# Kernel tuning notes

Hardware: AMD Instinct MI355X
Metric: run time of the kernel (lower is better)

Reference implementation:

```python
import jax, jax.numpy as jnp
import numpy as np

B, T, C, H = 2, 2048, 1024, 16
HS = C // H  # head size = 64


def _rope_cos_sin(t, hs):
    # theta_i = 1/10000^(2(i-1)/hs) for i in [1, hs/2]
    pos = jnp.arange(t, dtype=jnp.float32)[:, None]          # [T,1]
    i = jnp.arange(1, hs // 2 + 1, dtype=jnp.float32)[None]  # [1,hs/2]
    theta = 1.0 / 10000.0 ** (2.0 * (i - 1.0) / hs)
    ang = pos * theta                                        # [T,hs/2]
    return jnp.cos(ang), jnp.sin(ang)


def _apply_rope(u, cos, sin):
    # u: [B,H,T,HS]; complex multiply on consecutive pairs
    u2 = u.reshape(*u.shape[:-1], HS // 2, 2)
    x0, x1 = u2[..., 0], u2[..., 1]
    c = cos[None, None]  # [1,1,T,hs/2]
    s = sin[None, None]
    r0 = x0 * c - x1 * s
    r1 = x0 * s + x1 * c
    return jnp.stack([r0, r1], axis=-1).reshape(u.shape)


def setup_inputs() -> dict:
    key = jax.random.key(0)
    ks = jax.random.split(key, 5)
    return {
        "x": jax.random.normal(ks[0], (B, T, C), dtype=jnp.float32),
        "W_qkv": jax.random.normal(ks[1], (C, 3 * C), dtype=jnp.float32) * 0.02,
        "b_qkv": jax.random.normal(ks[2], (3 * C,), dtype=jnp.float32) * 0.02,
        "W_proj": jax.random.normal(ks[3], (C, C), dtype=jnp.float32) * 0.02,
        "b_proj": jax.random.normal(ks[4], (C,), dtype=jnp.float32) * 0.02,
    }


def reference(x, W_qkv, b_qkv, W_proj, b_proj):
    b, t, c = x.shape
    qkv = x @ W_qkv + b_qkv                                   # [B,T,3C]
    qkv = qkv.reshape(b, t, H, 3 * HS).transpose(0, 2, 1, 3)  # [B,H,T,3*HS]
    q, k, v = jnp.split(qkv, 3, axis=-1)                      # each [B,H,T,HS]

    cos, sin = _rope_cos_sin(t, HS)
    q = _apply_rope(q, cos, sin)
    k = _apply_rope(k, cos, sin)

    att = jnp.einsum("bhqd,bhkd->bhqk", q, k) / jnp.sqrt(jnp.float32(HS))
    causal = jnp.tril(jnp.ones((t, t), dtype=bool))[None, None]
    att = jnp.where(causal, att, jnp.float32(-1e9))
    att = jax.nn.softmax(att, axis=-1)
    y = jnp.einsum("bhqk,bhkd->bhqd", att, v)                 # [B,H,T,HS]
    y = y.transpose(0, 2, 1, 3).reshape(b, t, c)
    return y @ W_proj + b_proj
```

## Files before the change

kernel.cpp:

```cpp
#include <hip/hip_runtime.h>

typedef unsigned short u16;
typedef unsigned int u32;
typedef __bf16 bf16x8 __attribute__((ext_vector_type(8)));
typedef float f32x4 __attribute__((ext_vector_type(4)));
typedef float f32x16 __attribute__((ext_vector_type(16)));
typedef u32 u32x4 __attribute__((ext_vector_type(4)));
typedef u16 u16x4 __attribute__((ext_vector_type(4)));
typedef u16 u16x8 __attribute__((ext_vector_type(8)));

__device__ __forceinline__ u16 f2bf(float f) {
  u32 u = __builtin_bit_cast(u32, f);
  u += 0x7fffu + ((u >> 16) & 1u);
  return (u16)(u >> 16);
}

__device__ __forceinline__ u32 pk2(float a, float b) {
  u32 ua = __builtin_bit_cast(u32, a) + 0x8000u;
  u32 ub = __builtin_bit_cast(u32, b) + 0x8000u;
  return __builtin_amdgcn_perm(ub, ua, 0x07060302);
}

__device__ __forceinline__ void gld16(const void* g, void* l) {
  __builtin_amdgcn_global_load_lds(
      (const __attribute__((address_space(1))) void*)g,
      (__attribute__((address_space(3))) void*)l, 16, 0, 0);
}

__global__ __launch_bounds__(256) void k_prep(
    const float* __restrict__ x, u16* __restrict__ xb,
    const float* __restrict__ Wqkv, u16* __restrict__ Wqkvt,
    const float* __restrict__ Wproj, u16* __restrict__ Wpt,
    float2* __restrict__ rope) {
  __shared__ float tile[32][33];
  const int tid = threadIdx.x;
  int bx = blockIdx.x;
  if (bx < 4096) {
    int i = (bx * 256 + tid) * 4;
    float4 v = *(const float4*)(x + i);
    u16x4 o = { f2bf(v.x), f2bf(v.y), f2bf(v.z), f2bf(v.w) };
    *(u16x4*)(xb + i) = o;
    return;
  }
  bx -= 4096;
  const float* src; u16* dst; int R, Cc, bxx, byy;
  if (bx < 3072) {
    src = Wqkv; dst = Wqkvt; R = 1024; Cc = 3072; bxx = bx % 96; byy = bx / 96;
  } else if (bx < 4096) {
    int b = bx - 3072;
    src = Wproj; dst = Wpt; R = 1024; Cc = 1024; bxx = b % 32; byy = b / 32;
  } else {
    int i = (bx - 4096) * 256 + tid;
    int t = i >> 5, d = i & 31;
    float theta = expf(-(float)d * 0.28782313662425575f);
    float ang = (float)t * theta;
    rope[i] = make_float2(cosf(ang), sinf(ang));
    return;
  }
  int xx = tid & 31, yy = tid >> 5;
  int c0 = bxx * 32, r0 = byy * 32;
  for (int i = 0; i < 4; ++i)
    tile[yy + 8 * i][xx] = src[(size_t)(r0 + yy + 8 * i) * Cc + c0 + xx];
  __syncthreads();
  for (int i = 0; i < 4; ++i)
    dst[(size_t)(c0 + yy + 8 * i) * R + r0 + xx] = f2bf(tile[xx][yy + 8 * i]);
}

__global__ __launch_bounds__(256, 4) void k_qkv(
    const u16* __restrict__ Xb,
    const u16* __restrict__ Wt,
    const float* __restrict__ bias,
    const float2* __restrict__ rope,
    u16* __restrict__ Qg,
    u16* __restrict__ Kg,
    u16* __restrict__ Vt) {
  __shared__ alignas(16) u16 smem[18432];
  u16* As = smem;
  u16* Bs = smem + 8192;
  const int tid = threadIdx.x;
  const int lane = tid & 63, w = tid >> 6;
  const int quad = lane >> 4, l15 = lane & 15;
  const int m0 = blockIdx.y * 128, n0 = blockIdx.x * 128;
  const int wm = (w & 1) * 64, wn = (w >> 1) * 64;
  const int srow = lane >> 3, sj = lane & 7;
  const int sw = (sj ^ srow) * 8;
  const f32x4 vzero = {0.f, 0.f, 0.f, 0.f};

  f32x4 acc[4][4];
  for (int i = 0; i < 4; ++i)
    for (int j = 0; j < 4; ++j) acc[i][j] = vzero;

  for (int kt = 0; kt < 1024; kt += 64) {
    __syncthreads();
    for (int i = 0; i < 4; ++i) {
      int row = w * 32 + i * 8;
      gld16(Xb + (size_t)(m0 + row + srow) * 1024 + kt + sw, &As[row * 64]);
      gld16(Wt + (size_t)(n0 + row + srow) * 1024 + kt + sw, &Bs[row * 64]);
    }
    __syncthreads();
    for (int ks = 0; ks < 2; ++ks) {
      const int cc = ((ks * 4 + quad) ^ (l15 & 7)) * 8;
      bf16x8 a[4], b[4];
      for (int mt = 0; mt < 4; ++mt)
        a[mt] = *(const bf16x8*)&As[(wm + mt * 16 + l15) * 64 + cc];
      for (int nt = 0; nt < 4; ++nt)
        b[nt] = *(const bf16x8*)&Bs[(wn + nt * 16 + l15) * 64 + cc];
      for (int nt = 0; nt < 4; ++nt)
        for (int mt = 0; mt < 4; ++mt)
          acc[nt][mt] = __builtin_amdgcn_mfma_f32_16x16x32_bf16(
              b[nt], a[mt], acc[nt][mt], 0, 0, 0);
    }
  }
  __syncthreads();

  const int half = w >> 1;
  const int nh = n0 + half * 64;
  const int region = (nh % 192) >> 6;
  u16* Eh = smem + half * 9216;
  if (region < 2) {
    const float qsc = (region == 0) ? 0.18033688011112042f : 1.0f;
    for (int nt = 0; nt < 4; ++nt) {
      float4 bv4 = *(const float4*)&bias[nh + nt * 16 + quad * 4];
      for (int mt = 0; mt < 4; ++mt) {
        int m_l = wm + mt * 16 + l15;
        int t = (m0 + m_l) & 2047;
        float4 cs = *(const float4*)&rope[t * 32 + nt * 8 + quad * 2];
        float v0 = acc[nt][mt][0] + bv4.x;
        float v1 = acc[nt][mt][1] + bv4.y;
        float v2 = acc[nt][mt][2] + bv4.z;
        float v3 = acc[nt][mt][3] + bv4.w;
        float r0 = fmaf(-v1, cs.y, v0 * cs.x) * qsc;
        float r1 = fmaf( v0, cs.y, v1 * cs.x) * qsc;
        float r2 = fmaf(-v3, cs.w, v2 * cs.z) * qsc;
        float r3 = fmaf( v2, cs.w, v3 * cs.z) * qsc;
        uint2 pv; pv.x = pk2(r0, r1); pv.y = pk2(r2, r3);
        *(uint2*)&Eh[m_l * 72 + nt * 16 + quad * 4] = pv;
      }
    }
  } else {
    for (int nt = 0; nt < 4; ++nt) {
      float4 bv4 = *(const float4*)&bias[nh + nt * 16 + quad * 4];
      for (int mt = 0; mt < 4; ++mt) {
        int m_l = wm + mt * 16 + l15;
        int cb = nt * 16 + quad * 4;
        Eh[(cb + 0) * 136 + m_l] = f2bf(acc[nt][mt][0] + bv4.x);
        Eh[(cb + 1) * 136 + m_l] = f2bf(acc[nt][mt][1] + bv4.y);
        Eh[(cb + 2) * 136 + m_l] = f2bf(acc[nt][mt][2] + bv4.z);
        Eh[(cb + 3) * 136 + m_l] = f2bf(acc[nt][mt][3] + bv4.w);
      }
    }
  }
  __syncthreads();

  const int bb = m0 >> 11, t0 = m0 & 2047;
  for (int hf = 0; hf < 2; ++hf) {
    const int nhf = n0 + hf * 64;
    const int hh = nhf / 192;
    const int reg = (nhf % 192) >> 6;
    const u16* Ef = smem + hf * 9216;
    if (reg < 2) {
      u16* dst = (reg == 0 ? Qg : Kg) +
                 ((size_t)(bb * 16 + hh) * 2048 + t0) * 64;
      int chunk = tid & 7, row0 = tid >> 3;
      for (int p = 0; p < 4; ++p) {
        int row = row0 + p * 32;
        u16x8 val = *(const u16x8*)&Ef[row * 72 + chunk * 8];
        *(u16x8*)(dst + (size_t)row * 64 + chunk * 8) = val;
      }
    } else {
      u16* dstv = Vt + (size_t)(bb * 16 + hh) * 64 * 2048 + t0;
      int mch = tid & 15, c0r = tid >> 4;
      for (int p = 0; p < 4; ++p) {
        int c = c0r + p * 16;
        u16x8 val = *(const u16x8*)&Ef[c * 136 + mch * 8];
        *(u16x8*)(dstv + (size_t)c * 2048 + mch * 8) = val;
      }
    }
  }
}

__global__ __launch_bounds__(256, 2) void k_attn(
    const u16* __restrict__ Qg, const u16* __restrict__ Kg,
    const u16* __restrict__ Vt, u16* __restrict__ Og) {
  __shared__ alignas(16) u16 Ks[2][64 * 64];
  __shared__ alignas(16) u16 Vs[2][64 * 64];
  __shared__ float Ls[4][32];
  const int tid = threadIdx.x, lane = tid & 63, w = tid >> 6;
  const int q32 = lane & 31, hi = lane >> 5;
  const int id = blockIdx.x;
  const int xr = id & 7, j = id >> 3;
  const int bh = (j >> 3) * 8 + xr;
  const int tA = j & 7, tB = 15 - tA;
  const int nkbA = 2 * tA + 2;
  const u16* Qh = Qg + (size_t)bh * 2048 * 64;
  const u16* Kh = Kg + (size_t)bh * 2048 * 64;
  const u16* Vh = Vt + (size_t)bh * 64 * 2048;
  const int bb = bh >> 4, h = bh & 15;

  const int r8 = lane >> 3, j8 = lane & 7;
  const int sw_c = (j8 ^ r8) * 8;

  auto stage = [&](int i, int b) {
    const int kk0 = (i < nkbA ? i : i - nkbA) * 64;
    for (int t = 0; t < 2; ++t) {
      int row = w * 16 + t * 8;
      gld16(Kh + (size_t)(kk0 + row + r8) * 64 + sw_c, &Ks[b][row * 64]);
      gld16(Vh + (size_t)(row + r8) * 2048 + kk0 + sw_c, &Vs[b][row * 64]);
    }
  };

  bf16x8 aq[4];
  {
    const u16* qp = Qh + (size_t)(tA * 128 + w * 32 + q32) * 64 + hi * 8;
#pragma unroll
    for (int ds = 0; ds < 4; ++ds) aq[ds] = *(const bf16x8*)(qp + ds * 16);
  }
  asm volatile("" ::: "memory");
  stage(0, 0);
  stage(1, 1);

  f32x16 O0 = {}, O1 = {};
  float lsum = 0.f;
  int qb = tA * 128;
  int kcap = 2 * tA + (w >> 1);

  for (int it = 0; it < 34; ++it) {
    const int buf = it & 1;
    if (it == 33) asm volatile("s_waitcnt vmcnt(0)" ::: "memory");
    else          asm volatile("s_waitcnt vmcnt(4)" ::: "memory");
    asm volatile("s_barrier" ::: "memory");

    const bool isA = it < nkbA;
    const int kb = isA ? it : it - nkbA;

    if (kb <= kcap) {
      const int k0 = kb * 64;
      f32x16 st0 = {}, st1 = {};
#pragma unroll
      for (int ds = 0; ds < 4; ++ds) {
        const int c = ((ds * 2 + hi) ^ (q32 & 7)) * 8;
        bf16x8 ak0 = *(const bf16x8*)&Ks[buf][q32 * 64 + c];
        bf16x8 ak1 = *(const bf16x8*)&Ks[buf][(32 + q32) * 64 + c];
        st0 = __builtin_amdgcn_mfma_f32_32x32x16_bf16(ak0, aq[ds], st0, 0, 0, 0);
        st1 = __builtin_amdgcn_mfma_f32_32x32x16_bf16(ak1, aq[ds], st1, 0, 0, 0);
      }

      float p0[16], p1[16];
      if (kb == kcap) {
        const int q = qb + w * 32 + q32;
#pragma unroll
        for (int r = 0; r < 16; ++r) {
          int kk = k0 + (r & 3) + 8 * (r >> 2) + 4 * hi;
          float e0 = __builtin_amdgcn_exp2f(st0[r]);
          float e1 = __builtin_amdgcn_exp2f(st1[r]);
          p0[r] = (kk <= q) ? e0 : 0.f;
          p1[r] = (kk + 32 <= q) ? e1 : 0.f;
          lsum += p0[r] + p1[r];
        }
      } else {
#pragma unroll
        for (int r = 0; r < 16; ++r) {
          p0[r] = __builtin_amdgcn_exp2f(st0[r]);
          p1[r] = __builtin_amdgcn_exp2f(st1[r]);
          lsum += p0[r] + p1[r];
        }
      }

      u32 paw[4][4];
#pragma unroll
      for (int kt = 0; kt < 2; ++kt) {
        const float* P = kt ? p1 : p0;
#pragma unroll
        for (int kl = 0; kl < 2; ++kl) {
          const int b0i = kl * 8;
          u32 a0 = pk2(P[b0i + 0], P[b0i + 1]);
          u32 b0 = pk2(P[b0i + 4], P[b0i + 5]);
          u32 a1 = pk2(P[b0i + 2], P[b0i + 3]);
          u32 b1 = pk2(P[b0i + 6], P[b0i + 7]);
          asm volatile("v_permlane32_swap_b32 %0, %1" : "+v"(a0), "+v"(b0));
          asm volatile("v_permlane32_swap_b32 %0, %1" : "+v"(a1), "+v"(b1));
          const int s = kt * 2 + kl;
          paw[s][0] = a0; paw[s][1] = a1; paw[s][2] = b0; paw[s][3] = b1;
        }
      }

#pragma unroll
      for (int s = 0; s < 4; ++s) {
        u32x4 pw = { paw[s][0], paw[s][1], paw[s][2], paw[s][3] };
        bf16x8 pa = __builtin_bit_cast(bf16x8, pw);
        const int c = ((s * 2 + hi) ^ (q32 & 7)) * 8;
        bf16x8 bv0 = *(const bf16x8*)&Vs[buf][q32 * 64 + c];
        bf16x8 bv1 = *(const bf16x8*)&Vs[buf][(32 + q32) * 64 + c];
        O0 = __builtin_amdgcn_mfma_f32_32x32x16_bf16(pa, bv0, O0, 0, 0, 0);
        O1 = __builtin_amdgcn_mfma_f32_32x32x16_bf16(pa, bv1, O1, 0, 0, 0);
      }
    }

    asm volatile("s_barrier" ::: "memory");
    if (it + 2 < 34) stage(it + 2, buf);

    if (it == nkbA - 1) {
      float lt = lsum + __shfl_xor(lsum, 32, 64);
      float invl = 1.0f / lt;
      if (lane < 32) Ls[w][q32] = invl;
      u16* dst = Og + ((size_t)bb * 2048 + tA * 128 + w * 32) * 1024 + h * 64 + q32;
#pragma unroll
      for (int r = 0; r < 16; ++r) {
        int qp = (r & 3) + 8 * (r >> 2) + 4 * hi;
        float iv = Ls[w][qp];
        dst[(size_t)qp * 1024]      = f2bf(O0[r] * iv);
        dst[(size_t)qp * 1024 + 32] = f2bf(O1[r] * iv);
      }
      lsum = 0.f;
      O0 = {}; O1 = {};
      const u16* qp = Qh + (size_t)(tB * 128 + w * 32 + q32) * 64 + hi * 8;
#pragma unroll
      for (int ds = 0; ds < 4; ++ds) aq[ds] = *(const bf16x8*)(qp + ds * 16);
      qb = tB * 128;
      kcap = 2 * tB + (w >> 1);
    }
  }

  {
    float lt = lsum + __shfl_xor(lsum, 32, 64);
    float invl = 1.0f / lt;
    if (lane < 32) Ls[w][q32] = invl;
    u16* dst = Og + ((size_t)bb * 2048 + tB * 128 + w * 32) * 1024 + h * 64 + q32;
#pragma unroll
    for (int r = 0; r < 16; ++r) {
      int qp = (r & 3) + 8 * (r >> 2) + 4 * hi;
      float iv = Ls[w][qp];
      dst[(size_t)qp * 1024]      = f2bf(O0[r] * iv);
      dst[(size_t)qp * 1024 + 32] = f2bf(O1[r] * iv);
    }
  }
}

__global__ __launch_bounds__(256, 4) void k_proj(
    const u16* __restrict__ Ag,
    const u16* __restrict__ Wt,
    const float* __restrict__ bias,
    float* __restrict__ out) {
  __shared__ alignas(16) u16 As[64 * 64];
  __shared__ alignas(16) u16 Bs[128 * 64];
  const int tid = threadIdx.x;
  const int lane = tid & 63, w = tid >> 6;
  const int quad = lane >> 4, l15 = lane & 15;
  const int m0 = blockIdx.y * 64, n0 = blockIdx.x * 128;
  const int wm = (w & 1) * 32, wn = (w >> 1) * 64;
  const int srow = lane >> 3, sj = lane & 7;
  const int sw = (sj ^ srow) * 8;
  const f32x4 vzero = {0.f, 0.f, 0.f, 0.f};

  f32x4 acc[2][4];
  for (int i = 0; i < 2; ++i)
    for (int j = 0; j < 4; ++j) acc[i][j] = vzero;

  for (int kt = 0; kt < 1024; kt += 64) {
    __syncthreads();
    for (int i = 0; i < 2; ++i) {
      int row = w * 16 + i * 8;
      gld16(Ag + (size_t)(m0 + row + srow) * 1024 + kt + sw, &As[row * 64]);
    }
    for (int i = 0; i < 4; ++i) {
      int row = w * 32 + i * 8;
      gld16(Wt + (size_t)(n0 + row + srow) * 1024 + kt + sw, &Bs[row * 64]);
    }
    __syncthreads();
    for (int ks = 0; ks < 2; ++ks) {
      const int cc = ((ks * 4 + quad) ^ (l15 & 7)) * 8;
      bf16x8 a[2], b[4];
      for (int mt = 0; mt < 2; ++mt)
        a[mt] = *(const bf16x8*)&As[(wm + mt * 16 + l15) * 64 + cc];
      for (int nt = 0; nt < 4; ++nt)
        b[nt] = *(const bf16x8*)&Bs[(wn + nt * 16 + l15) * 64 + cc];
      for (int mt = 0; mt < 2; ++mt)
        for (int nt = 0; nt < 4; ++nt)
          acc[mt][nt] = __builtin_amdgcn_mfma_f32_16x16x32_bf16(
              a[mt], b[nt], acc[mt][nt], 0, 0, 0);
    }
  }

  for (int nt = 0; nt < 4; ++nt) {
    int n = n0 + wn + nt * 16 + l15;
    float bv = bias[n];
    for (int mt = 0; mt < 2; ++mt)
      for (int r = 0; r < 4; ++r) {
        int m = m0 + wm + mt * 16 + quad * 4 + r;
        out[(size_t)m * 1024 + n] = acc[mt][nt][r] + bv;
      }
  }
}

extern "C" void kernel_launch(void* const* d_in, const int* in_sizes, int n_in,
                              void* d_out, int out_size, void* d_ws, size_t ws_size,
                              hipStream_t stream) {
  (void)in_sizes; (void)n_in; (void)out_size; (void)ws_size;
  const float* x     = (const float*)d_in[0];
  const float* Wqkv  = (const float*)d_in[1];
  const float* bqkv  = (const float*)d_in[2];
  const float* Wproj = (const float*)d_in[3];
  const float* bproj = (const float*)d_in[4];
  float* out = (float*)d_out;

  char* ws = (char*)d_ws;
  size_t off = 0;
  u16* Xb    = (u16*)(ws + off); off += (size_t)4096 * 1024 * 2;
  u16* Wqkvt = (u16*)(ws + off); off += (size_t)3072 * 1024 * 2;
  u16* Wpt   = (u16*)(ws + off); off += (size_t)1024 * 1024 * 2;
  u16* Qg    = (u16*)(ws + off); off += (size_t)2 * 16 * 2048 * 64 * 2;
  u16* Kg    = (u16*)(ws + off); off += (size_t)2 * 16 * 2048 * 64 * 2;
  u16* Vt    = (u16*)(ws + off); off += (size_t)2 * 16 * 64 * 2048 * 2;
  u16* Att   = (u16*)(ws + off); off += (size_t)4096 * 1024 * 2;
  float2* rope = (float2*)(ws + off); off += (size_t)2048 * 32 * sizeof(float2);

  k_prep<<<8448, 256, 0, stream>>>(x, Xb, Wqkv, Wqkvt, Wproj, Wpt, rope);
  k_qkv<<<dim3(24, 32), 256, 0, stream>>>(Xb, Wqkvt, bqkv, rope, Qg, Kg, Vt);
  k_attn<<<256, 256, 0, stream>>>(Qg, Kg, Vt, Att);
  k_proj<<<dim3(8, 64), 256, 0, stream>>>(Att, Wpt, bproj, out);
}
```

Baseline: 171.3 us.

## Split paired causal tiles into separate blocks, heavy tiles first

The attention kernel previously had each block process two query tiles (t and 15-t) back to back, which balances causal work per block. Now each block handles a single 128-row query tile and the grid doubles to 512 blocks. Blocks are ordered so the long tiles (t=15..8) launch first and the short ones fill in afterwards. This gives more parallelism across the GPU's compute units. In exchange, each block does less work to amortise its Q loads and pipeline startup, and scheduling becomes less balanced.

After: 170.3 us. About the same (-0.6%).

```diff
diff --git a/kernel.cpp b/kernel.cpp
--- a/kernel.cpp
+++ b/kernel.cpp
@@ -188,10 +188,12 @@
   const int tid = threadIdx.x, lane = tid & 63, w = tid >> 6;
   const int q32 = lane & 31, hi = lane >> 5;
   const int id = blockIdx.x;
-  const int xr = id & 7, j = id >> 3;
-  const int bh = (j >> 3) * 8 + xr;
-  const int tA = j & 7, tB = 15 - tA;
-  const int nkbA = 2 * tA + 2;
+  const int xr = id & 7, m = id >> 3;
+  int t, grp;
+  if (m < 32) { t = 15 - (m & 7); grp = m >> 3; }
+  else        { int mm = m - 32; t = 7 - (mm & 7); grp = mm >> 3; }
+  const int bh = grp * 8 + xr;
+  const int nkb = 2 * t + 2;
   const u16* Qh = Qg + (size_t)bh * 2048 * 64;
   const u16* Kh = Kg + (size_t)bh * 2048 * 64;
   const u16* Vh = Vt + (size_t)bh * 64 * 2048;
@@ -201,9 +203,9 @@
   const int sw_c = (j8 ^ r8) * 8;
 
   auto stage = [&](int i, int b) {
-    const int kk0 = (i < nkbA ? i : i - nkbA) * 64;
-    for (int t = 0; t < 2; ++t) {
-      int row = w * 16 + t * 8;
+    const int kk0 = i * 64;
+    for (int tt = 0; tt < 2; ++tt) {
+      int row = w * 16 + tt * 8;
       gld16(Kh + (size_t)(kk0 + row + r8) * 64 + sw_c, &Ks[b][row * 64]);
       gld16(Vh + (size_t)(row + r8) * 2048 + kk0 + sw_c, &Vs[b][row * 64]);
     }
@@ -211,7 +213,7 @@
 
   bf16x8 aq[4];
   {
-    const u16* qp = Qh + (size_t)(tA * 128 + w * 32 + q32) * 64 + hi * 8;
+    const u16* qp = Qh + (size_t)(t * 128 + w * 32 + q32) * 64 + hi * 8;
 #pragma unroll
     for (int ds = 0; ds < 4; ++ds) aq[ds] = *(const bf16x8*)(qp + ds * 16);
   }
@@ -221,18 +223,15 @@
 
   f32x16 O0 = {}, O1 = {};
   float lsum = 0.f;
-  int qb = tA * 128;
-  int kcap = 2 * tA + (w >> 1);
-
-  for (int it = 0; it < 34; ++it) {
+  const int kcap = 2 * t + (w >> 1);
+
+  for (int it = 0; it < nkb; ++it) {
     const int buf = it & 1;
-    if (it == 33) asm volatile("s_waitcnt vmcnt(0)" ::: "memory");
-    else          asm volatile("s_waitcnt vmcnt(4)" ::: "memory");
+    if (it == nkb - 1) asm volatile("s_waitcnt vmcnt(0)" ::: "memory");
+    else               asm volatile("s_waitcnt vmcnt(4)" ::: "memory");
     asm volatile("s_barrier" ::: "memory");
 
-    const bool isA = it < nkbA;
-    const int kb = isA ? it : it - nkbA;
-
+    const int kb = it;
     if (kb <= kcap) {
       const int k0 = kb * 64;
       f32x16 st0 = {}, st1 = {};
@@ -247,7 +246,7 @@
 
       float p0[16], p1[16];
       if (kb == kcap) {
-        const int q = qb + w * 32 + q32;
+        const int q = t * 128 + w * 32 + q32;
 #pragma unroll
         for (int r = 0; r < 16; ++r) {
           int kk = k0 + (r & 3) + 8 * (r >> 2) + 4 * hi;
@@ -297,35 +296,14 @@
     }
 
     asm volatile("s_barrier" ::: "memory");
-    if (it + 2 < 34) stage(it + 2, buf);
-
-    if (it == nkbA - 1) {
-      float lt = lsum + __shfl_xor(lsum, 32, 64);
-      float invl = 1.0f / lt;
-      if (lane < 32) Ls[w][q32] = invl;
-      u16* dst = Og + ((size_t)bb * 2048 + tA * 128 + w * 32) * 1024 + h * 64 + q32;
-#pragma unroll
-      for (int r = 0; r < 16; ++r) {
-        int qp = (r & 3) + 8 * (r >> 2) + 4 * hi;
-        float iv = Ls[w][qp];
-        dst[(size_t)qp * 1024]      = f2bf(O0[r] * iv);
-        dst[(size_t)qp * 1024 + 32] = f2bf(O1[r] * iv);
-      }
-      lsum = 0.f;
-      O0 = {}; O1 = {};
-      const u16* qp = Qh + (size_t)(tB * 128 + w * 32 + q32) * 64 + hi * 8;
-#pragma unroll
-      for (int ds = 0; ds < 4; ++ds) aq[ds] = *(const bf16x8*)(qp + ds * 16);
-      qb = tB * 128;
-      kcap = 2 * tB + (w >> 1);
-    }
+    if (it + 2 < nkb) stage(it + 2, buf);
   }
 
   {
     float lt = lsum + __shfl_xor(lsum, 32, 64);
     float invl = 1.0f / lt;
     if (lane < 32) Ls[w][q32] = invl;
-    u16* dst = Og + ((size_t)bb * 2048 + tB * 128 + w * 32) * 1024 + h * 64 + q32;
+    u16* dst = Og + ((size_t)bb * 2048 + t * 128 + w * 32) * 1024 + h * 64 + q32;
 #pragma unroll
     for (int r = 0; r < 16; ++r) {
       int qp = (r & 3) + 8 * (r >> 2) + 4 * hi;
@@ -416,6 +394,6 @@
 
   k_prep<<<8448, 256, 0, stream>>>(x, Xb, Wqkv, Wqkvt, Wproj, Wpt, rope);
   k_qkv<<<dim3(24, 32), 256, 0, stream>>>(Xb, Wqkvt, bqkv, rope, Qg, Kg, Vt);
-  k_attn<<<256, 256, 0, stream>>>(Qg, Kg, Vt, Att);
+  k_attn<<<512, 256, 0, stream>>>(Qg, Kg, Vt, Att);
   k_proj<<<dim3(8, 64), 256, 0, stream>>>(Att, Wpt, bproj, out);
 }
```
